# Kernel tuning notes

Hardware: AMD Instinct MI355X
Metric: run time of the kernel (lower is better)

Reference implementation:

```python
import jax, jax.numpy as jnp
import numpy as np

B, T, N = 32, 2048, 2048
D, L, TE, H = 512, 256, 1024, 8

def _ln(x, g, b, eps=1e-5):
    m = x.mean(-1, keepdims=True)
    v = ((x - m) ** 2).mean(-1, keepdims=True)
    return (x - m) / jnp.sqrt(v + eps) * g + b

def setup_inputs() -> dict:
    key = jax.random.key(0)
    ks = jax.random.split(key, 12)
    s = 0.02
    return {
        "x": jax.random.normal(ks[0], (B, T, D), jnp.float32),
        "xf": jax.random.normal(ks[1], (B, N, L), jnp.float32),
        "emb": jax.random.normal(ks[2], (B, TE), jnp.float32),
        "norm_g": jnp.ones((D,), jnp.float32),
        "norm_b": jnp.zeros((D,), jnp.float32),
        "tnorm_g": jnp.ones((L,), jnp.float32),
        "tnorm_b": jnp.zeros((L,), jnp.float32),
        "Wq": jax.random.normal(ks[3], (D, D), jnp.float32) * s,
        "bq": jnp.zeros((D,), jnp.float32),
        "Wk": jax.random.normal(ks[4], (L, D), jnp.float32) * s,
        "bk": jnp.zeros((D,), jnp.float32),
        "Wv": jax.random.normal(ks[5], (L, D), jnp.float32) * s,
        "bv": jnp.zeros((D,), jnp.float32),
        "We": jax.random.normal(ks[6], (TE, 2 * D), jnp.float32) * s,
        "be": jnp.zeros((2 * D,), jnp.float32),
        "snorm_g": jnp.ones((D,), jnp.float32),
        "snorm_b": jnp.zeros((D,), jnp.float32),
        "Wo": jax.random.normal(ks[7], (D, D), jnp.float32) * s,
        "bo": jnp.zeros((D,), jnp.float32),
    }

def reference(x, xf, emb, norm_g, norm_b, tnorm_g, tnorm_b, Wq, bq, Wk, bk, Wv, bv,
              We, be, snorm_g, snorm_b, Wo, bo):
    b, t, d = x.shape
    n = xf.shape[1]
    hd = d // H
    # projections with pre-LayerNorms
    q = (_ln(x, norm_g, norm_b) @ Wq + bq).reshape(b, t, H, hd)
    xfn = _ln(xf, tnorm_g, tnorm_b)
    k = (xfn @ Wk + bk).reshape(b, n, H, hd)
    v = (xfn @ Wv + bv).reshape(b, n, H, hd)
    # dual softmax of linear attention: query over head-dim, key over sequence
    q = jax.nn.softmax(q, axis=-1)
    k = jax.nn.softmax(k, axis=1)
    # O(N*d^2) linear attention
    attn = jnp.einsum('bnhd,bnhl->bhdl', k, v)          # [B,H,hd,hd]
    y = jnp.einsum('bthd,bhdl->bthl', q, attn).reshape(b, t, d)
    # StylizationBlock (dropout is identity in eval)
    emb_out = jax.nn.silu(emb) @ We + be                # [B, 2D]
    scale, shift = emb_out[:, None, :d], emb_out[:, None, d:]
    h = _ln(y, snorm_g, snorm_b) * (1.0 + scale) + shift
    h = jax.nn.silu(h) @ Wo + bo
    return x + h
```

## Files before the change

### kernel.cpp

```cpp
#include <hip/hip_runtime.h>
#include <math.h>

#define B_ 32
#define T_ 2048
#define N_ 2048
#define D_ 512
#define L_ 256
#define TE_ 1024
#define H_ 8
#define MROWS 65536
#define KCH 16
#define NC_ 8

typedef __attribute__((ext_vector_type(8))) short short8;
typedef __attribute__((ext_vector_type(4))) float f32x4;
typedef __attribute__((ext_vector_type(4))) unsigned short us4;

__device__ __forceinline__ unsigned short f2bf(float f) {
  unsigned u = __float_as_uint(f);
  unsigned r = (u + 0x7FFF + ((u >> 16) & 1)) >> 16;
  return (unsigned short)r;
}
__device__ __forceinline__ float bf2f(unsigned short u) {
  return __uint_as_float(((unsigned)u) << 16);
}
__device__ __forceinline__ void gload_lds16(const void* g, void* l) {
  __builtin_amdgcn_global_load_lds(
      (const __attribute__((address_space(1))) void*)g,
      (__attribute__((address_space(3))) void*)l, 16, 0, 0);
}

__device__ __forceinline__ float blockReduceSum(float v, float* ws) {
#pragma unroll
  for (int m = 32; m >= 1; m >>= 1) v += __shfl_xor(v, m, 64);
  int wid = threadIdx.x >> 6;
  int lane = threadIdx.x & 63;
  __syncthreads();
  if (lane == 0) ws[wid] = v;
  __syncthreads();
  return ws[0] + ws[1] + ws[2] + ws[3];
}

template <int COLS>
__global__ void __launch_bounds__(256) ln_rows(const float* __restrict__ in,
                                               const float* __restrict__ g,
                                               const float* __restrict__ bb,
                                               unsigned short* __restrict__ out) {
  constexpr int E = COLS / 256;
  __shared__ float ws[4];
  size_t row = blockIdx.x;
  const float* rp = in + row * COLS;
  float v[E];
  float s = 0.f;
#pragma unroll
  for (int e = 0; e < E; ++e) {
    v[e] = rp[threadIdx.x + e * 256];
    s += v[e];
  }
  s = blockReduceSum(s, ws);
  float mean = s * (1.0f / COLS);
  float q = 0.f;
#pragma unroll
  for (int e = 0; e < E; ++e) {
    float d = v[e] - mean;
    q += d * d;
  }
  q = blockReduceSum(q, ws);
  float rstd = rsqrtf(q * (1.0f / COLS) + 1e-5f);
  unsigned short* op = out + row * COLS;
#pragma unroll
  for (int e = 0; e < E; ++e) {
    int c = threadIdx.x + e * 256;
    op[c] = f2bf((v[e] - mean) * rstd * g[c] + bb[c]);
  }
}

__global__ void __launch_bounds__(256) transcast_all(const float* __restrict__ Wq,
                                                     const float* __restrict__ Wk,
                                                     const float* __restrict__ Wv,
                                                     const float* __restrict__ Wo,
                                                     unsigned short* __restrict__ wqt,
                                                     unsigned short* __restrict__ wkt,
                                                     unsigned short* __restrict__ wvt,
                                                     unsigned short* __restrict__ wot) {
  int z = blockIdx.z;
  const float* W;
  unsigned short* Wt;
  int K;
  if (z == 0) { W = Wq; Wt = wqt; K = 512; }
  else if (z == 1) { W = Wk; Wt = wkt; K = 256; }
  else if (z == 2) { W = Wv; Wt = wvt; K = 256; }
  else { W = Wo; Wt = wot; K = 512; }
  int k0 = blockIdx.x * 32, n0 = blockIdx.y * 32;
  if (k0 >= K) return;
  __shared__ float t[32][33];
  int tx = threadIdx.x & 31, ty = threadIdx.x >> 5;
#pragma unroll
  for (int i = 0; i < 32; i += 8)
    t[ty + i][tx] = W[(size_t)(k0 + ty + i) * 512 + n0 + tx];
  __syncthreads();
#pragma unroll
  for (int i = 0; i < 32; i += 8)
    Wt[(size_t)(n0 + ty + i) * K + k0 + tx] = f2bf(t[tx][ty + i]);
}

template <int KT, bool ADD, bool OUTBF, bool QSM, bool KSTATS>
__global__ void __launch_bounds__(256) gemm_mfma(const unsigned short* __restrict__ A,
                                                 const unsigned short* __restrict__ Wt,
                                                 const float* __restrict__ bias,
                                                 const float* __restrict__ add,
                                                 void* __restrict__ Cv,
                                                 float* __restrict__ pmaxO,
                                                 float* __restrict__ psumO) {
  __shared__ __align__(16) unsigned short sA[2][128 * 32];
  __shared__ __align__(16) unsigned short sB[2][128 * 32];
  int tid = threadIdx.x;
  int w = tid >> 6, lane = tid & 63;
  int quad = lane >> 4, r16 = lane & 15;
  int wr = w >> 1, wc = w & 1;
  size_t m0 = (size_t)blockIdx.y * 128;
  int n0 = blockIdx.x * 128;
  int srow = lane >> 2;
  int scol = (lane & 3) * 8;
  f32x4 acc[4][4] = {};

  const unsigned short* Arow0 = &A[(m0 + w * 32 + srow) * KT + scol];
  const unsigned short* Brow0 = &Wt[(size_t)(n0 + w * 32 + srow) * KT + scol];

#define G_STAGE(buf, k0)                                                          \
  do {                                                                            \
    gload_lds16(Arow0 + (k0), &sA[buf][(w * 2 + 0) * 512]);                       \
    gload_lds16(Arow0 + (size_t)16 * KT + (k0), &sA[buf][(w * 2 + 1) * 512]);     \
    gload_lds16(Brow0 + (k0), &sB[buf][(w * 2 + 0) * 512]);                       \
    gload_lds16(Brow0 + (size_t)16 * KT + (k0), &sB[buf][(w * 2 + 1) * 512]);     \
  } while (0)

#define G_COMPUTE(buf)                                                            \
  do {                                                                            \
    short8 af[4], bfr[4];                                                         \
    _Pragma("unroll") for (int mi = 0; mi < 4; ++mi)                              \
        af[mi] = *(const short8*)&sA[buf][(wr * 64 + mi * 16 + r16) * 32 + quad * 8]; \
    _Pragma("unroll") for (int ni = 0; ni < 4; ++ni)                              \
        bfr[ni] = *(const short8*)&sB[buf][(wc * 64 + ni * 16 + r16) * 32 + quad * 8]; \
    _Pragma("unroll") for (int mi = 0; mi < 4; ++mi)                              \
        _Pragma("unroll") for (int ni = 0; ni < 4; ++ni)                          \
            acc[mi][ni] =                                                         \
                __builtin_amdgcn_mfma_f32_16x16x32_bf16(af[mi], bfr[ni], acc[mi][ni], 0, 0, 0); \
  } while (0)

  constexpr int NT = KT / 32;
  G_STAGE(0, 0);
  __syncthreads();
#pragma unroll 1
  for (int t = 0; t < NT; t += 2) {
    if (t + 1 < NT) G_STAGE(1, (t + 1) * 32);
    G_COMPUTE(0);
    __syncthreads();
    if (t + 2 < NT) G_STAGE(0, (t + 2) * 32);
    G_COMPUTE(1);
    __syncthreads();
  }
#undef G_STAGE
#undef G_COMPUTE

  float* Cf = (float*)Cv;
  unsigned short* Cb = (unsigned short*)Cv;

  if constexpr (QSM) {
#pragma unroll
    for (int mi = 0; mi < 4; ++mi)
#pragma unroll
      for (int r = 0; r < 4; ++r) {
        size_t grow = m0 + wr * 64 + mi * 16 + quad * 4 + r;
        float v4[4];
        float mx = -1e30f;
#pragma unroll
        for (int ni = 0; ni < 4; ++ni) {
          v4[ni] = acc[mi][ni][r] + bias[n0 + wc * 64 + ni * 16 + r16];
          mx = fmaxf(mx, v4[ni]);
        }
#pragma unroll
        for (int s = 8; s >= 1; s >>= 1) mx = fmaxf(mx, __shfl_xor(mx, s, 64));
        float ssum = 0.f;
#pragma unroll
        for (int ni = 0; ni < 4; ++ni) {
          v4[ni] = expf(v4[ni] - mx);
          ssum += v4[ni];
        }
#pragma unroll
        for (int s = 8; s >= 1; s >>= 1) ssum += __shfl_xor(ssum, s, 64);
        float inv = 1.f / ssum;
#pragma unroll
        for (int ni = 0; ni < 4; ++ni) {
          int gcol = n0 + wc * 64 + ni * 16 + r16;
          Cb[grow * 512 + gcol] = f2bf(v4[ni] * inv);
        }
      }
  } else if constexpr (KSTATS) {
    float tmax[4], tsum[4];
#pragma unroll
    for (int ni = 0; ni < 4; ++ni) { tmax[ni] = -1e30f; tsum[ni] = 0.f; }
#pragma unroll
    for (int mi = 0; mi < 4; ++mi)
#pragma unroll
      for (int r = 0; r < 4; ++r) {
        size_t grow = m0 + wr * 64 + mi * 16 + quad * 4 + r;
#pragma unroll
        for (int ni = 0; ni < 4; ++ni) {
          int gcol = n0 + wc * 64 + ni * 16 + r16;
          unsigned short bv = f2bf(acc[mi][ni][r] + bias[gcol]);
          Cb[grow * 512 + gcol] = bv;
          tmax[ni] = fmaxf(tmax[ni], bf2f(bv));
        }
      }
#pragma unroll
    for (int mi = 0; mi < 4; ++mi)
#pragma unroll
      for (int r = 0; r < 4; ++r)
#pragma unroll
        for (int ni = 0; ni < 4; ++ni) {
          int gcol = n0 + wc * 64 + ni * 16 + r16;
          float vr = bf2f(f2bf(acc[mi][ni][r] + bias[gcol]));
          tsum[ni] += expf(vr - tmax[ni]);
        }
#pragma unroll
    for (int ni = 0; ni < 4; ++ni) {
#pragma unroll
      for (int mask = 16; mask <= 32; mask <<= 1) {
        float om = __shfl_xor(tmax[ni], mask, 64);
        float os = __shfl_xor(tsum[ni], mask, 64);
        float nm = fmaxf(tmax[ni], om);
        tsum[ni] = tsum[ni] * expf(tmax[ni] - nm) + os * expf(om - nm);
        tmax[ni] = nm;
      }
    }
    __shared__ float smax[4][64], ssum2[4][64];
    if (quad == 0) {
#pragma unroll
      for (int ni = 0; ni < 4; ++ni) {
        smax[w][ni * 16 + r16] = tmax[ni];
        ssum2[w][ni * 16 + r16] = tsum[ni];
      }
    }
    __syncthreads();
    if (w < 2 && quad == 0) {
      int b = (int)(blockIdx.y >> 4), ch = (int)(blockIdx.y & 15);
#pragma unroll
      for (int ni = 0; ni < 4; ++ni) {
        int i = ni * 16 + r16;
        float m1 = smax[w][i], m2 = smax[w + 2][i];
        float s1 = ssum2[w][i], s2 = ssum2[w + 2][i];
        float nm = fmaxf(m1, m2);
        float ss = s1 * expf(m1 - nm) + s2 * expf(m2 - nm);
        size_t off = ((size_t)(b * KCH + ch)) * D_ + n0 + w * 64 + i;
        pmaxO[off] = nm;
        psumO[off] = ss;
      }
    }
  } else {
#pragma unroll
    for (int mi = 0; mi < 4; ++mi)
#pragma unroll
      for (int r = 0; r < 4; ++r) {
        size_t grow = m0 + wr * 64 + mi * 16 + quad * 4 + r;
#pragma unroll
        for (int ni = 0; ni < 4; ++ni) {
          int gcol = n0 + wc * 64 + ni * 16 + r16;
          float val = acc[mi][ni][r] + bias[gcol];
          if constexpr (ADD) val += add[grow * 512 + gcol];
          if constexpr (OUTBF)
            Cb[grow * 512 + gcol] = f2bf(val);
          else
            Cf[grow * 512 + gcol] = val;
        }
      }
  }
}

__global__ void __launch_bounds__(256) attn_part_kernel(const unsigned short* __restrict__ k,
                                                        const unsigned short* __restrict__ v,
                                                        const float* __restrict__ pmax,
                                                        const float* __restrict__ psum,
                                                        float* __restrict__ part) {
  int b = blockIdx.x, h = blockIdx.y, nc = blockIdx.z;
  int tid = threadIdx.x;
  __shared__ float ks_[32][68];
  __shared__ float vs_[32][68];
  __shared__ float mx[64], is_[64];
  int lr = tid >> 4;
  int c4 = (tid & 15) * 4;
  const unsigned short* kp = k + ((size_t)b * N_ + nc * 256) * D_ + h * 64;
  const unsigned short* vp = v + ((size_t)b * N_ + nc * 256) * D_ + h * 64;
  us4 kv0 = *(const us4*)&kp[(size_t)lr * D_ + c4];
  us4 vv0 = *(const us4*)&vp[(size_t)lr * D_ + c4];
  us4 kv1 = *(const us4*)&kp[(size_t)(lr + 16) * D_ + c4];
  us4 vv1 = *(const us4*)&vp[(size_t)(lr + 16) * D_ + c4];
  if (tid < 64) {
    int c = h * 64 + tid;
    float m = -1e30f, s = 0.f;
#pragma unroll
    for (int ch = 0; ch < KCH; ++ch) {
      float pm = pmax[((size_t)(b * KCH + ch)) * D_ + c];
      float ps = psum[((size_t)(b * KCH + ch)) * D_ + c];
      float nm = fmaxf(m, pm);
      s = s * expf(m - nm) + ps * expf(pm - nm);
      m = nm;
    }
    mx[tid] = m;
    is_[tid] = 1.f / s;
  }
  float acc[4][4] = {};
  int tx = tid & 15, ty = tid >> 4;
  for (int n0 = 0; n0 < 256; n0 += 32) {
    __syncthreads();
#pragma unroll
    for (int j = 0; j < 4; ++j) {
      ks_[lr][c4 + j] = expf(bf2f(kv0[j]) - mx[c4 + j]) * is_[c4 + j];
      vs_[lr][c4 + j] = bf2f(vv0[j]);
      ks_[lr + 16][c4 + j] = expf(bf2f(kv1[j]) - mx[c4 + j]) * is_[c4 + j];
      vs_[lr + 16][c4 + j] = bf2f(vv1[j]);
    }
    if (n0 + 32 < 256) {
      kv0 = *(const us4*)&kp[(size_t)(n0 + 32 + lr) * D_ + c4];
      vv0 = *(const us4*)&vp[(size_t)(n0 + 32 + lr) * D_ + c4];
      kv1 = *(const us4*)&kp[(size_t)(n0 + 48 + lr) * D_ + c4];
      vv1 = *(const us4*)&vp[(size_t)(n0 + 48 + lr) * D_ + c4];
    }
    __syncthreads();
#pragma unroll
    for (int nn = 0; nn < 32; ++nn) {
      float av[4], bv2[4];
#pragma unroll
      for (int i = 0; i < 4; ++i) av[i] = ks_[nn][ty * 4 + i];
#pragma unroll
      for (int j = 0; j < 4; ++j) bv2[j] = vs_[nn][tx * 4 + j];
#pragma unroll
      for (int i = 0; i < 4; ++i)
#pragma unroll
        for (int j = 0; j < 4; ++j) acc[i][j] += av[i] * bv2[j];
    }
  }
  float* ap = part + ((size_t)(b * H_ + h) * NC_ + nc) * 4096;
#pragma unroll
  for (int i = 0; i < 4; ++i) {
    float4 st = make_float4(acc[i][0], acc[i][1], acc[i][2], acc[i][3]);
    *(float4*)&ap[(ty * 4 + i) * 64 + tx * 4] = st;
  }
}

__global__ void __launch_bounds__(256) attn_reduce(const float* __restrict__ part,
                                                   unsigned short* __restrict__ attnT) {
  size_t o = ((size_t)blockIdx.x * 256 + threadIdx.x) * 4;
  size_t bh = o >> 12;
  size_t e = o & 4095;
  float4 s = make_float4(0.f, 0.f, 0.f, 0.f);
#pragma unroll
  for (int nc = 0; nc < NC_; ++nc) {
    float4 p = *(const float4*)&part[(bh * NC_ + nc) * 4096 + e];
    s.x += p.x;
    s.y += p.y;
    s.z += p.z;
    s.w += p.w;
  }
  int d = (int)(e >> 6);
  int l = (int)(e & 63);
  unsigned short* ab = attnT + bh * 4096;
  ab[(l + 0) * 64 + d] = f2bf(s.x);
  ab[(l + 1) * 64 + d] = f2bf(s.y);
  ab[(l + 2) * 64 + d] = f2bf(s.z);
  ab[(l + 3) * 64 + d] = f2bf(s.w);
}

__global__ void __launch_bounds__(256) embmod(const float* __restrict__ emb,
                                              const float* __restrict__ We,
                                              const float* __restrict__ be,
                                              float* __restrict__ eo) {
  int b = blockIdx.x, tid = threadIdx.x;
  __shared__ float se[TE_];
  for (int i = tid; i < TE_; i += 256) {
    float e = emb[b * TE_ + i];
    se[i] = e / (1.f + expf(-e));
  }
  __syncthreads();
  int j0 = tid * 4;
  float a0 = 0, a1 = 0, a2 = 0, a3 = 0;
  for (int i = 0; i < TE_; ++i) {
    float s = se[i];
    float4 wv = *(const float4*)&We[(size_t)i * 1024 + j0];
    a0 += s * wv.x;
    a1 += s * wv.y;
    a2 += s * wv.z;
    a3 += s * wv.w;
  }
  eo[b * 1024 + j0 + 0] = a0 + be[j0 + 0];
  eo[b * 1024 + j0 + 1] = a1 + be[j0 + 1];
  eo[b * 1024 + j0 + 2] = a2 + be[j0 + 2];
  eo[b * 1024 + j0 + 3] = a3 + be[j0 + 3];
}

__global__ void __launch_bounds__(256) yein_mfma(const unsigned short* __restrict__ qsm,
                                                 const unsigned short* __restrict__ attnT,
                                                 float* __restrict__ y) {
  int b = blockIdx.z, h = blockIdx.y;
  size_t t0 = (size_t)blockIdx.x * 256;
  int tid = threadIdx.x;
  int w = tid >> 6, lane = tid & 63;
  int quad = lane >> 4, r16 = lane & 15;
  int srow = lane >> 2;
  int scol = (lane & 3) * 8;
  __shared__ __align__(16) unsigned short sA[2][256 * 32];
  __shared__ __align__(16) unsigned short sB[2][64 * 32];
  const unsigned short* qp = qsm + ((size_t)b * T_ + t0) * D_ + h * 64;
  const unsigned short* bp = attnT + (size_t)(b * H_ + h) * 4096;
  f32x4 acc[4][4] = {};

#pragma unroll
  for (int half = 0; half < 2; ++half) {
    int k0 = half * 32;
#pragma unroll
    for (int i = 0; i < 4; ++i) {
      int seg = w * 4 + i;
      gload_lds16(&qp[(size_t)(seg * 16 + srow) * D_ + k0 + scol], &sA[half][seg * 512]);
    }
    gload_lds16(&bp[(w * 16 + srow) * 64 + k0 + scol], &sB[half][w * 512]);
  }
  __syncthreads();
#pragma unroll
  for (int half = 0; half < 2; ++half) {
    short8 af[4], bfr[4];
#pragma unroll
    for (int mi = 0; mi < 4; ++mi)
      af[mi] = *(const short8*)&sA[half][(w * 64 + mi * 16 + r16) * 32 + quad * 8];
#pragma unroll
    for (int ni = 0; ni < 4; ++ni)
      bfr[ni] = *(const short8*)&sB[half][(ni * 16 + r16) * 32 + quad * 8];
#pragma unroll
    for (int mi = 0; mi < 4; ++mi)
#pragma unroll
      for (int ni = 0; ni < 4; ++ni)
        acc[mi][ni] = __builtin_amdgcn_mfma_f32_16x16x32_bf16(af[mi], bfr[ni], acc[mi][ni], 0, 0, 0);
  }

#pragma unroll
  for (int mi = 0; mi < 4; ++mi)
#pragma unroll
    for (int r = 0; r < 4; ++r) {
      size_t grow = t0 + w * 64 + mi * 16 + quad * 4 + r;
      float* yp = y + ((size_t)b * T_ + grow) * D_ + h * 64;
#pragma unroll
      for (int ni = 0; ni < 4; ++ni) yp[ni * 16 + r16] = acc[mi][ni][r];
    }
}

__global__ void __launch_bounds__(256) modln(const float* __restrict__ y,
                                             const float* __restrict__ sg,
                                             const float* __restrict__ sb,
                                             const float* __restrict__ eo,
                                             unsigned short* __restrict__ hs) {
  __shared__ float ws[4];
  size_t row = blockIdx.x;
  int b = (int)(row >> 11);
  const float* rp = y + row * D_;
  float v[2];
  float s = 0.f;
#pragma unroll
  for (int e = 0; e < 2; ++e) {
    v[e] = rp[threadIdx.x + e * 256];
    s += v[e];
  }
  s = blockReduceSum(s, ws);
  float mean = s * (1.0f / D_);
  float q = 0.f;
#pragma unroll
  for (int e = 0; e < 2; ++e) {
    float d = v[e] - mean;
    q += d * d;
  }
  q = blockReduceSum(q, ws);
  float rstd = rsqrtf(q * (1.0f / D_) + 1e-5f);
#pragma unroll
  for (int e = 0; e < 2; ++e) {
    int c = threadIdx.x + e * 256;
    float xm = (v[e] - mean) * rstd * sg[c] + sb[c];
    float sc = eo[b * 1024 + c];
    float sh = eo[b * 1024 + D_ + c];
    float hm = xm * (1.f + sc) + sh;
    hs[row * D_ + c] = f2bf(hm / (1.f + expf(-hm)));
  }
}

extern "C" void kernel_launch(void* const* d_in, const int* in_sizes, int n_in,
                              void* d_out, int out_size, void* d_ws, size_t ws_size,
                              hipStream_t stream) {
  const float* x = (const float*)d_in[0];
  const float* xf = (const float*)d_in[1];
  const float* emb = (const float*)d_in[2];
  const float* norm_g = (const float*)d_in[3];
  const float* norm_b = (const float*)d_in[4];
  const float* tnorm_g = (const float*)d_in[5];
  const float* tnorm_b = (const float*)d_in[6];
  const float* Wq = (const float*)d_in[7];
  const float* bq = (const float*)d_in[8];
  const float* Wk = (const float*)d_in[9];
  const float* bk = (const float*)d_in[10];
  const float* Wv = (const float*)d_in[11];
  const float* bv = (const float*)d_in[12];
  const float* We = (const float*)d_in[13];
  const float* be = (const float*)d_in[14];
  const float* sg = (const float*)d_in[15];
  const float* sb = (const float*)d_in[16];
  const float* Wo = (const float*)d_in[17];
  const float* bo = (const float*)d_in[18];
  float* out = (float*)d_out;

  float* w = (float*)d_ws;
  unsigned short* qbf = (unsigned short*)w;
  unsigned short* kb = (unsigned short*)(w + 16777216);
  unsigned short* vb = (unsigned short*)(w + 33554432);
  float* ybuf = w + 50331648;
  unsigned short* xnbf = (unsigned short*)(w + 83886080);
  unsigned short* xfnbf = (unsigned short*)(w + 100663296);
  float* attnpart = w + 100663296;
  unsigned short* attnT = (unsigned short*)(w + 109051904);
  float* pmaxp = w + 109051904 + 524288;
  float* psump = pmaxp + 262144;
  float* embout = psump + 262144;
  unsigned short* wqt = (unsigned short*)(embout + 32768);
  unsigned short* wkt = wqt + 262144;
  unsigned short* wvt = wkt + 131072;
  unsigned short* wot = wvt + 131072;

  transcast_all<<<dim3(16, 16, 4), 256, 0, stream>>>(Wq, Wk, Wv, Wo, wqt, wkt, wvt, wot);
  ln_rows<512><<<MROWS, 256, 0, stream>>>(x, norm_g, norm_b, xnbf);
  gemm_mfma<512, false, true, true, false><<<dim3(4, 512), 256, 0, stream>>>(
      xnbf, wqt, bq, nullptr, qbf, nullptr, nullptr);
  ln_rows<256><<<MROWS, 256, 0, stream>>>(xf, tnorm_g, tnorm_b, xfnbf);
  gemm_mfma<256, false, true, false, true><<<dim3(4, 512), 256, 0, stream>>>(
      xfnbf, wkt, bk, nullptr, kb, pmaxp, psump);
  gemm_mfma<256, false, true, false, false><<<dim3(4, 512), 256, 0, stream>>>(
      xfnbf, wvt, bv, nullptr, vb, nullptr, nullptr);
  attn_part_kernel<<<dim3(32, 8, NC_), 256, 0, stream>>>(kb, vb, pmaxp, psump, attnpart);
  attn_reduce<<<1024, 256, 0, stream>>>(attnpart, attnT);
  embmod<<<32, 256, 0, stream>>>(emb, We, be, embout);
  yein_mfma<<<dim3(8, 8, 32), 256, 0, stream>>>(qbf, attnT, ybuf);
  modln<<<MROWS, 256, 0, stream>>>(ybuf, sg, sb, embout, xnbf);
  gemm_mfma<512, true, false, false, false><<<dim3(4, 512), 256, 0, stream>>>(
      xnbf, wot, bo, x, out, nullptr, nullptr);
}
```

Measured before the change: 904.5 us.

## Move query softmax into yein kernel and swizzle GEMM blocks across XCDs

The query head-dim softmax no longer runs in the Q-projection GEMM epilogue. Instead, yein_mfma computes it per row from the bf16 q tile in shared memory: it writes the unnormalized exponentials back to LDS and folds 1/sum into the output scaling. Separately, the GEMM block index is remapped so that consecutive M tiles are grouped per XCD, aiming to improve L2 locality. The cost is an extra LDS pass with 64 floats per thread in registers inside yein, plus rounding q to bf16 before the softmax is applied.

```diff
diff --git a/kernel.cpp b/kernel.cpp
--- a/kernel.cpp
+++ b/kernel.cpp
@@ -104,7 +104,7 @@
     Wt[(size_t)(n0 + ty + i) * K + k0 + tx] = f2bf(t[tx][ty + i]);
 }
 
-template <int KT, bool ADD, bool OUTBF, bool QSM, bool KSTATS>
+template <int KT, bool ADD, bool OUTBF, bool KSTATS>
 __global__ void __launch_bounds__(256) gemm_mfma(const unsigned short* __restrict__ A,
                                                  const unsigned short* __restrict__ Wt,
                                                  const float* __restrict__ bias,
@@ -118,8 +118,12 @@
   int w = tid >> 6, lane = tid & 63;
   int quad = lane >> 4, r16 = lane & 15;
   int wr = w >> 1, wc = w & 1;
-  size_t m0 = (size_t)blockIdx.y * 128;
-  int n0 = blockIdx.x * 128;
+  int s = blockIdx.x + (blockIdx.y << 2);
+  int xcd = s & 7, j = s >> 3;
+  int by = xcd * 64 + (j >> 2);
+  int bx = j & 3;
+  size_t m0 = (size_t)by * 128;
+  int n0 = bx * 128;
   int srow = lane >> 2;
   int scol = (lane & 3) * 8;
   f32x4 acc[4][4] = {};
@@ -166,37 +170,7 @@
   float* Cf = (float*)Cv;
   unsigned short* Cb = (unsigned short*)Cv;
 
-  if constexpr (QSM) {
-#pragma unroll
-    for (int mi = 0; mi < 4; ++mi)
-#pragma unroll
-      for (int r = 0; r < 4; ++r) {
-        size_t grow = m0 + wr * 64 + mi * 16 + quad * 4 + r;
-        float v4[4];
-        float mx = -1e30f;
-#pragma unroll
-        for (int ni = 0; ni < 4; ++ni) {
-          v4[ni] = acc[mi][ni][r] + bias[n0 + wc * 64 + ni * 16 + r16];
-          mx = fmaxf(mx, v4[ni]);
-        }
-#pragma unroll
-        for (int s = 8; s >= 1; s >>= 1) mx = fmaxf(mx, __shfl_xor(mx, s, 64));
-        float ssum = 0.f;
-#pragma unroll
-        for (int ni = 0; ni < 4; ++ni) {
-          v4[ni] = expf(v4[ni] - mx);
-          ssum += v4[ni];
-        }
-#pragma unroll
-        for (int s = 8; s >= 1; s >>= 1) ssum += __shfl_xor(ssum, s, 64);
-        float inv = 1.f / ssum;
-#pragma unroll
-        for (int ni = 0; ni < 4; ++ni) {
-          int gcol = n0 + wc * 64 + ni * 16 + r16;
-          Cb[grow * 512 + gcol] = f2bf(v4[ni] * inv);
-        }
-      }
-  } else if constexpr (KSTATS) {
+  if constexpr (KSTATS) {
     float tmax[4], tsum[4];
 #pragma unroll
     for (int ni = 0; ni < 4; ++ni) { tmax[ni] = -1e30f; tsum[ni] = 0.f; }
@@ -244,7 +218,7 @@
     }
     __syncthreads();
     if (w < 2 && quad == 0) {
-      int b = (int)(blockIdx.y >> 4), ch = (int)(blockIdx.y & 15);
+      int b = by >> 4, ch = by & 15;
 #pragma unroll
       for (int ni = 0; ni < 4; ++ni) {
         int i = ni * 16 + r16;
@@ -398,7 +372,7 @@
   eo[b * 1024 + j0 + 3] = a3 + be[j0 + 3];
 }
 
-__global__ void __launch_bounds__(256) yein_mfma(const unsigned short* __restrict__ qsm,
+__global__ void __launch_bounds__(256) yein_mfma(const unsigned short* __restrict__ q,
                                                  const unsigned short* __restrict__ attnT,
                                                  float* __restrict__ y) {
   int b = blockIdx.z, h = blockIdx.y;
@@ -410,7 +384,8 @@
   int scol = (lane & 3) * 8;
   __shared__ __align__(16) unsigned short sA[2][256 * 32];
   __shared__ __align__(16) unsigned short sB[2][64 * 32];
-  const unsigned short* qp = qsm + ((size_t)b * T_ + t0) * D_ + h * 64;
+  __shared__ float inv_s[256];
+  const unsigned short* qp = q + ((size_t)b * T_ + t0) * D_ + h * 64;
   const unsigned short* bp = attnT + (size_t)(b * H_ + h) * 4096;
   f32x4 acc[4][4] = {};
 
@@ -425,6 +400,42 @@
     gload_lds16(&bp[(w * 16 + srow) * 64 + k0 + scol], &sB[half][w * 512]);
   }
   __syncthreads();
+
+  {
+    int r = tid;
+    float vals[64];
+#pragma unroll
+    for (int hf = 0; hf < 2; ++hf)
+#pragma unroll
+      for (int blk = 0; blk < 4; ++blk) {
+        short8 vv = *(const short8*)&sA[hf][r * 32 + blk * 8];
+#pragma unroll
+        for (int jj = 0; jj < 8; ++jj)
+          vals[hf * 32 + blk * 8 + jj] = bf2f((unsigned short)vv[jj]);
+      }
+    float m = vals[0];
+#pragma unroll
+    for (int i = 1; i < 64; ++i) m = fmaxf(m, vals[i]);
+    float ssum = 0.f;
+#pragma unroll
+    for (int i = 0; i < 64; ++i) {
+      vals[i] = expf(vals[i] - m);
+      ssum += vals[i];
+    }
+    inv_s[r] = 1.f / ssum;
+#pragma unroll
+    for (int hf = 0; hf < 2; ++hf)
+#pragma unroll
+      for (int blk = 0; blk < 4; ++blk) {
+        short8 vv;
+#pragma unroll
+        for (int jj = 0; jj < 8; ++jj)
+          vv[jj] = (short)f2bf(vals[hf * 32 + blk * 8 + jj]);
+        *(short8*)&sA[hf][r * 32 + blk * 8] = vv;
+      }
+  }
+  __syncthreads();
+
 #pragma unroll
   for (int half = 0; half < 2; ++half) {
     short8 af[4], bfr[4];
@@ -445,10 +456,12 @@
   for (int mi = 0; mi < 4; ++mi)
 #pragma unroll
     for (int r = 0; r < 4; ++r) {
-      size_t grow = t0 + w * 64 + mi * 16 + quad * 4 + r;
+      int lrow = w * 64 + mi * 16 + quad * 4 + r;
+      float sc = inv_s[lrow];
+      size_t grow = t0 + lrow;
       float* yp = y + ((size_t)b * T_ + grow) * D_ + h * 64;
 #pragma unroll
-      for (int ni = 0; ni < 4; ++ni) yp[ni * 16 + r16] = acc[mi][ni][r];
+      for (int ni = 0; ni < 4; ++ni) yp[ni * 16 + r16] = acc[mi][ni][r] * sc;
     }
 }
 
@@ -532,18 +545,18 @@
 
   transcast_all<<<dim3(16, 16, 4), 256, 0, stream>>>(Wq, Wk, Wv, Wo, wqt, wkt, wvt, wot);
   ln_rows<512><<<MROWS, 256, 0, stream>>>(x, norm_g, norm_b, xnbf);
-  gemm_mfma<512, false, true, true, false><<<dim3(4, 512), 256, 0, stream>>>(
+  gemm_mfma<512, false, true, false><<<dim3(4, 512), 256, 0, stream>>>(
       xnbf, wqt, bq, nullptr, qbf, nullptr, nullptr);
   ln_rows<256><<<MROWS, 256, 0, stream>>>(xf, tnorm_g, tnorm_b, xfnbf);
-  gemm_mfma<256, false, true, false, true><<<dim3(4, 512), 256, 0, stream>>>(
+  gemm_mfma<256, false, true, true><<<dim3(4, 512), 256, 0, stream>>>(
       xfnbf, wkt, bk, nullptr, kb, pmaxp, psump);
-  gemm_mfma<256, false, true, false, false><<<dim3(4, 512), 256, 0, stream>>>(
+  gemm_mfma<256, false, true, false><<<dim3(4, 512), 256, 0, stream>>>(
       xfnbf, wvt, bv, nullptr, vb, nullptr, nullptr);
   attn_part_kernel<<<dim3(32, 8, NC_), 256, 0, stream>>>(kb, vb, pmaxp, psump, attnpart);
   attn_reduce<<<1024, 256, 0, stream>>>(attnpart, attnT);
   embmod<<<32, 256, 0, stream>>>(emb, We, be, embout);
   yein_mfma<<<dim3(8, 8, 32), 256, 0, stream>>>(qbf, attnT, ybuf);
   modln<<<MROWS, 256, 0, stream>>>(ybuf, sg, sb, embout, xnbf);
-  gemm_mfma<512, true, false, false, false><<<dim3(4, 512), 256, 0, stream>>>(
+  gemm_mfma<512, true, false, false><<<dim3(4, 512), 256, 0, stream>>>(
       xnbf, wot, bo, x, out, nullptr, nullptr);
 }
```

Measured after the change: 863.3 us. 1.05x faster.
